# Kernel tuning notes

Measured on AMD Instinct MI355X. Metric: run time of the kernel, lower is better.

Reference implementation:

```python
import jax, jax.numpy as jnp
import numpy as np

B, N, DN = 8, 4096, 64
E = 1048576
H, DM = 128, 64   # message MLP: 2*DN -> H -> DM
HU, F = 128, 64   # node-update MLP: DN+DM -> HU -> F


def setup_inputs() -> dict:
    key = jax.random.key(0)
    ks = jax.random.split(key, 13)
    inp = {
        'node_feats': jax.random.normal(ks[0], (B, N, DN), dtype=jnp.float32),
        'edge_b': jax.random.randint(ks[1], (E,), 0, B, dtype=jnp.int32),
        'edge_src': jax.random.randint(ks[2], (E,), 0, N, dtype=jnp.int32),
        'edge_dst': jax.random.randint(ks[3], (E,), 0, N, dtype=jnp.int32),
        'edge_vals': jax.random.uniform(ks[4], (E,), dtype=jnp.float32),
        # message MLP params (Dense-relu, Dense-linear)
        'Wm1': jax.random.normal(ks[5], (2 * DN, H), dtype=jnp.float32) / np.sqrt(2 * DN),
        'bm1': jnp.zeros((H,), jnp.float32),
        'Wm2': jax.random.normal(ks[6], (H, DM), dtype=jnp.float32) / np.sqrt(H),
        'bm2': jnp.zeros((DM,), jnp.float32),
        # node-update MLP params
        'Wu1': jax.random.normal(ks[7], (DN + DM, HU), dtype=jnp.float32) / np.sqrt(DN + DM),
        'bu1': jnp.zeros((HU,), jnp.float32),
        'Wu2': jax.random.normal(ks[8], (HU, F), dtype=jnp.float32) / np.sqrt(HU),
        'bu2': jnp.zeros((F,), jnp.float32),
    }
    return inp


def reference(node_feats, edge_b, edge_src, edge_dst, edge_vals,
              Wm1, bm1, Wm2, bm2, Wu1, bu1, Wu2, bu2):
    # --- create messages: gather src/target feats per edge ---
    src_feats = node_feats[edge_b, edge_src]            # (E, DN)
    tgt_feats = node_feats[edge_b, edge_dst]            # (E, DN)
    feats = jnp.concatenate([src_feats, tgt_feats], axis=-1)  # (E, 2*DN)
    h = jax.nn.relu(feats @ Wm1 + bm1)
    messages = h @ Wm2 + bm2                            # (E, DM)

    # --- gather (scatter) messages: weighted ragged segment-mean ---
    weighted = messages * edge_vals[:, None]            # (E, DM)
    seg = edge_b * N + edge_src                          # rowids b*max_N + src
    sums = jax.ops.segment_sum(weighted, seg, num_segments=B * N)
    counts = jax.ops.segment_sum(jnp.ones((E,), weighted.dtype), seg,
                                 num_segments=B * N)
    gathered = sums / jnp.maximum(counts, 1.0)[:, None]  # mean; 0 for empty rows
    gathered = gathered.reshape(B, N, DM)

    # --- update nodes ---
    upd_in = jnp.concatenate([node_feats, gathered], axis=-1)  # (B, N, DN+DM)
    hu = jax.nn.relu(upd_in @ Wu1 + bu1)
    updated = hu @ Wu2 + bu2                            # (B, N, F)
    return updated
```

## Files before the change

### kernel.cpp

```cpp
#include <hip/hip_runtime.h>

#define NB 8
#define NN 4096
#define DNF 64
#define NEDGE 1048576
#define DM 64
#define FF 64

#define NBKT2 2048
#define SPB2 16
#define NXCD 8
#define SUBCAP 192
#define OVFCAP 65536

using f32x4 = __attribute__((ext_vector_type(4))) float;
using s16x8 = __attribute__((ext_vector_type(8))) short;

__device__ __forceinline__ unsigned short f2b(float f) {
    union { float f; unsigned u; } v; v.f = f;
    unsigned r = (v.u + 0x7fffu + ((v.u >> 16) & 1u)) >> 16;
    return (unsigned short)r;
}
__device__ __forceinline__ float uif(unsigned u) {
    union { unsigned u; float f; } v; v.u = u;
    return v.f;
}

__device__ __forceinline__ void pack_one(const float* __restrict__ W,
                                         unsigned short* __restrict__ out,
                                         int K, int Ncols, int idx) {
    int j = idx & 7;
    int lane = (idx >> 3) & 63;
    int frag = idx >> 9;
    int KS = K >> 5;
    int ks = frag % KS;
    int nt = frag / KS;
    int k = ks * 32 + ((lane >> 4) << 3) + j;
    int col = nt * 16 + (lane & 15);
    out[idx] = f2b(W[k * Ncols + col]);
}

__global__ void pack_all(const float* __restrict__ Wm1, const float* __restrict__ Wm2,
                         const float* __restrict__ Wu1, const float* __restrict__ Wu2,
                         unsigned short* __restrict__ Qw, unsigned short* __restrict__ Pw,
                         unsigned short* __restrict__ Wm2p,
                         unsigned short* __restrict__ Wu1p, unsigned short* __restrict__ Wu2p) {
    int idx = blockIdx.x * 256 + threadIdx.x;
    if (idx < 8192)        pack_one(Wm1,              Qw,   64, 128, idx);
    else if (idx < 16384)  pack_one(Wm1 + 64 * 128,   Pw,   64, 128, idx - 8192);
    else if (idx < 24576)  pack_one(Wm2,              Wm2p, 128, 64, idx - 16384);
    else if (idx < 40960)  pack_one(Wu1,              Wu1p, 128, 128, idx - 24576);
    else                   pack_one(Wu2,              Wu2p, 128, 64, idx - 40960);
}

__global__ void pack_weights(const float* __restrict__ W, unsigned short* __restrict__ out,
                             int K, int Ncols) {
    int idx = blockIdx.x * 256 + threadIdx.x;
    if (idx >= K * Ncols) return;
    pack_one(W, out, K, Ncols, idx);
}

__launch_bounds__(256, 4)
__global__ void precompute_pq(const float* __restrict__ X,
                              const unsigned short* __restrict__ Qw,
                              const unsigned short* __restrict__ Pw,
                              const float* __restrict__ b1,
                              unsigned short* __restrict__ Qp,
                              unsigned short* __restrict__ Pp) {
    __shared__ unsigned short A[64][72];
    const int tid = threadIdx.x;
    const int g0 = blockIdx.x * 64;
    for (int i = 0; i < 16; ++i) {
        int idx = i * 256 + tid;
        int node = idx >> 6;
        int f = idx & 63;
        A[node][f] = f2b(X[(size_t)(g0 + node) * DNF + f]);
    }
    __syncthreads();
    const int wave = tid >> 6, lane = tid & 63;
    const int lr = lane & 15, lq = lane >> 4;
    const int arow = wave * 16 + lr;
    s16x8 a[2];
#pragma unroll
    for (int ks = 0; ks < 2; ++ks)
        a[ks] = *reinterpret_cast<const s16x8*>(&A[arow][ks * 32 + lq * 8]);
#pragma unroll
    for (int nt = 0; nt < 8; ++nt) {
        f32x4 accQ = {0.f, 0.f, 0.f, 0.f};
        f32x4 accP = {0.f, 0.f, 0.f, 0.f};
#pragma unroll
        for (int ks = 0; ks < 2; ++ks) {
            s16x8 bq = *reinterpret_cast<const s16x8*>(&Qw[(((nt << 1) + ks) * 64 + lane) * 8]);
            s16x8 bp = *reinterpret_cast<const s16x8*>(&Pw[(((nt << 1) + ks) * 64 + lane) * 8]);
            accQ = __builtin_amdgcn_mfma_f32_16x16x32_bf16(a[ks], bq, accQ, 0, 0, 0);
            accP = __builtin_amdgcn_mfma_f32_16x16x32_bf16(a[ks], bp, accP, 0, 0, 0);
        }
        int col = nt * 16 + lr;
        float bias = b1[col];
#pragma unroll
        for (int j = 0; j < 4; ++j) {
            int row = g0 + wave * 16 + lq * 4 + j;
            Qp[(size_t)row * 128 + col] = f2b(accQ[j] + bias);
            Pp[(size_t)row * 128 + col] = f2b(accP[j]);
        }
    }
}

__launch_bounds__(256, 8)
__global__ void scatter_xcd(const int* __restrict__ eb, const int* __restrict__ esrc,
                            const int* __restrict__ edst, const float* __restrict__ evals,
                            unsigned* __restrict__ gcurX, unsigned* __restrict__ payslot,
                            unsigned* __restrict__ ovf_cnt, unsigned* __restrict__ ovf_seg,
                            unsigned* __restrict__ ovf_pay) {
    unsigned xcd;
    asm volatile("s_getreg_b32 %0, hwreg(HW_REG_XCC_ID)" : "=s"(xcd));
    xcd &= (NXCD - 1);
    const int t0 = blockIdx.x * 1024 + threadIdx.x;
    int seg[4]; unsigned pk[4];
#pragma unroll
    for (int k = 0; k < 4; ++k) {
        int e = t0 + k * 256;
        seg[k] = eb[e] * NN + esrc[e];
        unsigned wq = (unsigned)fminf(evals[e] * 8192.0f + 0.5f, 8191.0f);
        pk[k] = (unsigned)edst[e] | (wq << 12) | ((unsigned)(seg[k] & 15) << 25);
    }
    unsigned pos[4];
#pragma unroll
    for (int k = 0; k < 4; ++k)
        pos[k] = atomicAdd(&gcurX[xcd * NBKT2 + (seg[k] >> 4)], 1u);
#pragma unroll
    for (int k = 0; k < 4; ++k) {
        if (pos[k] < (unsigned)SUBCAP) {
            payslot[((size_t)(seg[k] >> 4) * NXCD + xcd) * SUBCAP + pos[k]] = pk[k];
        } else {
            unsigned o = atomicAdd(ovf_cnt, 1u);
            if (o < (unsigned)OVFCAP) { ovf_seg[o] = (unsigned)seg[k]; ovf_pay[o] = pk[k]; }
        }
    }
}

__launch_bounds__(256, 6)
__global__ void bucket16_fused(const unsigned short* __restrict__ Qp,
                               const unsigned short* __restrict__ Pp,
                               const unsigned* __restrict__ payslot,
                               const unsigned* __restrict__ gcurX,
                               const unsigned* __restrict__ ovf_cnt,
                               const unsigned* __restrict__ ovf_seg,
                               const unsigned* __restrict__ ovf_pay,
                               const unsigned short* __restrict__ Wm2p,
                               const float* __restrict__ b2m,
                               const float* __restrict__ X,
                               const unsigned short* __restrict__ Wu1p,
                               const float* __restrict__ bu1,
                               const unsigned short* __restrict__ Wu2p,
                               const float* __restrict__ bu2,
                               float* __restrict__ out) {
    __shared__ unsigned sorted[NXCD * SUBCAP];
    __shared__ unsigned short S[16][136];
    __shared__ unsigned short A1[16][136];
    __shared__ unsigned short Hs[16][136];
    __shared__ unsigned h[16];
    __shared__ unsigned offs[17];
    __shared__ unsigned curb[16];
    __shared__ unsigned cx[NXCD];
    __shared__ float SW[16], SC[16];
    const int tid = threadIdx.x, wv = tid >> 6, lane = tid & 63;
    const int bkt = blockIdx.x;
    const int node0 = bkt * SPB2;
    const int rowbase = (bkt >> 8) << 12;
    const unsigned novf = ovf_cnt[0];

#pragma unroll
    for (int i = 0; i < 4; ++i) {
        int idx = i * 256 + tid;
        int row = idx >> 6, f = idx & 63;
        A1[row][f] = f2b(X[(size_t)(node0 + row) * DNF + f]);
    }
    if (tid < 16) h[tid] = 0;
    if (tid < NXCD) cx[tid] = min(gcurX[tid * NBKT2 + bkt], (unsigned)SUBCAP);
    __syncthreads();
    for (int x = 0; x < NXCD; ++x) {
        unsigned c = cx[x];
        for (unsigned i = tid; i < c; i += 256) {
            unsigned v = payslot[((size_t)bkt * NXCD + x) * SUBCAP + i];
            atomicAdd(&h[(v >> 25) & 15u], 1u);
        }
    }
    __syncthreads();
    if (tid < 16) {
        int xx = (int)h[tid];
#pragma unroll
        for (int o = 1; o < 16; o <<= 1) {
            int y = __shfl_up(xx, o);
            if (tid >= o) xx += y;
        }
        offs[tid + 1] = (unsigned)xx;
        if (tid == 0) offs[0] = 0;
    }
    __syncthreads();
    if (tid < 16) curb[tid] = offs[tid];
    __syncthreads();
    for (int x = 0; x < NXCD; ++x) {
        unsigned c = cx[x];
        for (unsigned i = tid; i < c; i += 256) {
            unsigned v = payslot[((size_t)bkt * NXCD + x) * SUBCAP + i];
            unsigned pos = atomicAdd(&curb[(v >> 25) & 15u], 1u);
            sorted[pos] = v;
        }
    }
    __syncthreads();

    const unsigned* P32 = reinterpret_cast<const unsigned*>(Pp);
    const unsigned* Q32 = reinterpret_cast<const unsigned*>(Qp);
    for (int si = 0; si < 4; ++si) {
        const int lo = wv * 4 + si;
        const int seg = node0 + lo;
        const unsigned s0 = offs[lo], s1 = offs[lo + 1];
        unsigned qv = Q32[(size_t)seg * 64 + lane];
        float q0 = uif(qv << 16);
        float q1 = uif(qv & 0xffff0000u);
        float acc0 = 0.f, acc1 = 0.f, wsum = 0.f;
        unsigned scnt = s1 - s0;

        for (unsigned bse = s0; bse < s1; bse += 8) {
            unsigned pv[8]; float wf[8];
#pragma unroll
            for (int k = 0; k < 8; ++k) {
                unsigned idx = bse + (unsigned)k;
                unsigned c = (idx < s1) ? sorted[idx] : 0u;
                wf[k] = (float)((c >> 12) & 8191u) * (1.0f / 8192.0f);
                pv[k] = P32[(size_t)(rowbase + (int)(c & 0xfffu)) * 64 + lane];
            }
#pragma unroll
            for (int k = 0; k < 8; ++k) {
                float p0 = uif(pv[k] << 16);
                float p1 = uif(pv[k] & 0xffff0000u);
                acc0 = fmaf(wf[k], fmaxf(q0 + p0, 0.f), acc0);
                acc1 = fmaf(wf[k], fmaxf(q1 + p1, 0.f), acc1);
                wsum += wf[k];
            }
        }
        if (novf > 0) {
            unsigned ncl = min(novf, (unsigned)OVFCAP);
            for (unsigned i = 0; i < ncl; ++i) {
                if (ovf_seg[i] == (unsigned)seg) {
                    unsigned c = ovf_pay[i];
                    float w = (float)((c >> 12) & 8191u) * (1.0f / 8192.0f);
                    unsigned pv = P32[(size_t)(rowbase + (int)(c & 0xfffu)) * 64 + lane];
                    acc0 = fmaf(w, fmaxf(q0 + uif(pv << 16), 0.f), acc0);
                    acc1 = fmaf(w, fmaxf(q1 + uif(pv & 0xffff0000u), 0.f), acc1);
                    wsum += w;
                    scnt += 1;
                }
            }
        }
        unsigned sp = (unsigned)f2b(acc0) | ((unsigned)f2b(acc1) << 16);
        *reinterpret_cast<unsigned*>(&S[lo][2 * lane]) = sp;
        if (lane == 0) {
            SW[lo] = wsum;
            SC[lo] = 1.0f / (float)max(scnt, 1u);
        }
    }
    __syncthreads();

    const int lr = lane & 15, lq = lane >> 4;
    {
        s16x8 a[4];
#pragma unroll
        for (int ks = 0; ks < 4; ++ks)
            a[ks] = *reinterpret_cast<const s16x8*>(&S[lr][ks * 32 + lq * 8]);
        f32x4 acc = {0.f, 0.f, 0.f, 0.f};
#pragma unroll
        for (int ks = 0; ks < 4; ++ks) {
            s16x8 bf = *reinterpret_cast<const s16x8*>(&Wm2p[(((wv << 2) + ks) * 64 + lane) * 8]);
            acc = __builtin_amdgcn_mfma_f32_16x16x32_bf16(a[ks], bf, acc, 0, 0, 0);
        }
        float bb = b2m[wv * 16 + lr];
#pragma unroll
        for (int j = 0; j < 4; ++j) {
            int r = lq * 4 + j;
            float g = (acc[j] + SW[r] * bb) * SC[r];
            A1[r][64 + wv * 16 + lr] = f2b(g);
        }
    }
    __syncthreads();

    {
        s16x8 a1[4];
#pragma unroll
        for (int ks = 0; ks < 4; ++ks)
            a1[ks] = *reinterpret_cast<const s16x8*>(&A1[lr][ks * 32 + lq * 8]);
#pragma unroll
        for (int t = 0; t < 2; ++t) {
            int nt = wv * 2 + t;
            f32x4 acc = {0.f, 0.f, 0.f, 0.f};
#pragma unroll
            for (int ks = 0; ks < 4; ++ks) {
                s16x8 bf = *reinterpret_cast<const s16x8*>(&Wu1p[(((nt << 2) + ks) * 64 + lane) * 8]);
                acc = __builtin_amdgcn_mfma_f32_16x16x32_bf16(a1[ks], bf, acc, 0, 0, 0);
            }
            float bias = bu1[nt * 16 + lr];
#pragma unroll
            for (int j = 0; j < 4; ++j) {
                float hh = fmaxf(acc[j] + bias, 0.f);
                Hs[lq * 4 + j][nt * 16 + lr] = f2b(hh);
            }
        }
    }
    __syncthreads();

    {
        s16x8 a2[4];
#pragma unroll
        for (int ks = 0; ks < 4; ++ks)
            a2[ks] = *reinterpret_cast<const s16x8*>(&Hs[lr][ks * 32 + lq * 8]);
        f32x4 acc = {0.f, 0.f, 0.f, 0.f};
#pragma unroll
        for (int ks = 0; ks < 4; ++ks) {
            s16x8 bf = *reinterpret_cast<const s16x8*>(&Wu2p[(((wv << 2) + ks) * 64 + lane) * 8]);
            acc = __builtin_amdgcn_mfma_f32_16x16x32_bf16(a2[ks], bf, acc, 0, 0, 0);
        }
        float bias = bu2[wv * 16 + lr];
#pragma unroll
        for (int j = 0; j < 4; ++j)
            out[(size_t)(node0 + lq * 4 + j) * FF + wv * 16 + lr] = acc[j] + bias;
    }
}


template<int SCALE>
__launch_bounds__(256, 4)
__global__ void node_kernel(const float* __restrict__ node_feats,
                            const float* __restrict__ sums, const float* __restrict__ counts,
                            const unsigned short* __restrict__ W1p, const float* __restrict__ b1,
                            const unsigned short* __restrict__ W2p, const float* __restrict__ b2,
                            float* __restrict__ out) {
    __shared__ unsigned short A1[64][136];
    __shared__ unsigned short Hs[64][136];
    const int tid = threadIdx.x;
    const int g0 = blockIdx.x * 64;
    for (int i = 0; i < 16; ++i) {
        int idx = i * 256 + tid;
        int node = idx >> 6;
        int p = idx & 63;
        int g = g0 + node;
        float2 v;
        if (p < 32) {
            v = *reinterpret_cast<const float2*>(node_feats + (size_t)g * DNF + 2 * p);
        } else {
            float2 s = *reinterpret_cast<const float2*>(sums + (size_t)g * DM + 2 * p - 64);
            if (SCALE) {
                float scale = 1.0f / fmaxf(counts[g], 1.0f);
                s.x *= scale; s.y *= scale;
            }
            v = s;
        }
        unsigned packed = (unsigned)f2b(v.x) | ((unsigned)f2b(v.y) << 16);
        *reinterpret_cast<unsigned*>(&A1[node][2 * p]) = packed;
    }
    __syncthreads();
    const int wave = tid >> 6, lane = tid & 63;
    const int lr = lane & 15, lq = lane >> 4;
    const int arow = wave * 16 + lr;
    s16x8 a[4];
#pragma unroll
    for (int ks = 0; ks < 4; ++ks)
        a[ks] = *reinterpret_cast<const s16x8*>(&A1[arow][ks * 32 + lq * 8]);
#pragma unroll
    for (int nt = 0; nt < 8; ++nt) {
        f32x4 acc = {0.f, 0.f, 0.f, 0.f};
#pragma unroll
        for (int ks = 0; ks < 4; ++ks) {
            s16x8 bf = *reinterpret_cast<const s16x8*>(&W1p[(((nt << 2) + ks) * 64 + lane) * 8]);
            acc = __builtin_amdgcn_mfma_f32_16x16x32_bf16(a[ks], bf, acc, 0, 0, 0);
        }
        float bias = b1[nt * 16 + lr];
#pragma unroll
        for (int j = 0; j < 4; ++j) {
            float h = acc[j] + bias;
            h = h > 0.f ? h : 0.f;
            Hs[wave * 16 + lq * 4 + j][nt * 16 + lr] = f2b(h);
        }
    }
    s16x8 a2[4];
#pragma unroll
    for (int ks = 0; ks < 4; ++ks)
        a2[ks] = *reinterpret_cast<const s16x8*>(&Hs[arow][ks * 32 + lq * 8]);
#pragma unroll
    for (int nt = 0; nt < 4; ++nt) {
        f32x4 acc = {0.f, 0.f, 0.f, 0.f};
#pragma unroll
        for (int ks = 0; ks < 4; ++ks) {
            s16x8 bf = *reinterpret_cast<const s16x8*>(&W2p[(((nt << 2) + ks) * 64 + lane) * 8]);
            acc = __builtin_amdgcn_mfma_f32_16x16x32_bf16(a2[ks], bf, acc, 0, 0, 0);
        }
        float bias = b2[nt * 16 + lr];
#pragma unroll
        for (int j = 0; j < 4; ++j) {
            int g = g0 + wave * 16 + lq * 4 + j;
            out[(size_t)g * FF + nt * 16 + lr] = acc[j] + bias;
        }
    }
}

__launch_bounds__(256, 4)
__global__ void edge_kernel(const float* __restrict__ node_feats,
                            const int* __restrict__ eb, const int* __restrict__ esrc,
                            const int* __restrict__ edst, const float* __restrict__ evals,
                            const unsigned short* __restrict__ W1p, const float* __restrict__ b1,
                            const unsigned short* __restrict__ W2p, const float* __restrict__ b2,
                            float* __restrict__ sums, float* __restrict__ counts) {
    __shared__ unsigned short A1[64][136];
    __shared__ unsigned short Hs[64][136];
    const int tid = threadIdx.x;
    const int e0 = blockIdx.x * 64;
    if (tid < 64) {
        int e = e0 + tid;
        atomicAdd(&counts[eb[e] * NN + esrc[e]], 1.0f);
    }
    for (int i = 0; i < 16; ++i) {
        int idx = i * 256 + tid;
        int edge = idx >> 6;
        int p = idx & 63;
        int e = e0 + edge;
        int b = eb[e];
        const float* row;
        if (p < 32) row = node_feats + ((size_t)b * NN + esrc[e]) * DNF;
        else        row = node_feats + ((size_t)b * NN + edst[e]) * DNF - 64;
        float2 v = *reinterpret_cast<const float2*>(row + 2 * p);
        unsigned packed = (unsigned)f2b(v.x) | ((unsigned)f2b(v.y) << 16);
        *reinterpret_cast<unsigned*>(&A1[edge][2 * p]) = packed;
    }
    __syncthreads();
    const int wave = tid >> 6, lane = tid & 63;
    const int lr = lane & 15, lq = lane >> 4;
    const int arow = wave * 16 + lr;
    s16x8 a[4];
#pragma unroll
    for (int ks = 0; ks < 4; ++ks)
        a[ks] = *reinterpret_cast<const s16x8*>(&A1[arow][ks * 32 + lq * 8]);
#pragma unroll
    for (int nt = 0; nt < 8; ++nt) {
        f32x4 acc = {0.f, 0.f, 0.f, 0.f};
#pragma unroll
        for (int ks = 0; ks < 4; ++ks) {
            s16x8 bf = *reinterpret_cast<const s16x8*>(&W1p[(((nt << 2) + ks) * 64 + lane) * 8]);
            acc = __builtin_amdgcn_mfma_f32_16x16x32_bf16(a[ks], bf, acc, 0, 0, 0);
        }
        float bias = b1[nt * 16 + lr];
#pragma unroll
        for (int j = 0; j < 4; ++j) {
            float h = acc[j] + bias;
            h = h > 0.f ? h : 0.f;
            Hs[wave * 16 + lq * 4 + j][nt * 16 + lr] = f2b(h);
        }
    }
    s16x8 a2[4];
#pragma unroll
    for (int ks = 0; ks < 4; ++ks)
        a2[ks] = *reinterpret_cast<const s16x8*>(&Hs[arow][ks * 32 + lq * 8]);
    float ev[4]; int seg4[4];
#pragma unroll
    for (int j = 0; j < 4; ++j) {
        int r = e0 + wave * 16 + lq * 4 + j;
        ev[j] = evals[r];
        seg4[j] = eb[r] * NN + esrc[r];
    }
#pragma unroll
    for (int nt = 0; nt < 4; ++nt) {
        f32x4 acc = {0.f, 0.f, 0.f, 0.f};
#pragma unroll
        for (int ks = 0; ks < 4; ++ks) {
            s16x8 bf = *reinterpret_cast<const s16x8*>(&W2p[(((nt << 2) + ks) * 64 + lane) * 8]);
            acc = __builtin_amdgcn_mfma_f32_16x16x32_bf16(a2[ks], bf, acc, 0, 0, 0);
        }
        float bias = b2[nt * 16 + lr];
#pragma unroll
        for (int j = 0; j < 4; ++j) {
            float m = (acc[j] + bias) * ev[j];
            atomicAdd(&sums[(size_t)seg4[j] * DM + nt * 16 + lr], m);
        }
    }
}

extern "C" void kernel_launch(void* const* d_in, const int* in_sizes, int n_in,
                              void* d_out, int out_size, void* d_ws, size_t ws_size,
                              hipStream_t stream) {
    const float* node_feats = (const float*)d_in[0];
    const int*   eb    = (const int*)d_in[1];
    const int*   esrc  = (const int*)d_in[2];
    const int*   edst  = (const int*)d_in[3];
    const float* evals = (const float*)d_in[4];
    const float* Wm1 = (const float*)d_in[5];
    const float* bm1 = (const float*)d_in[6];
    const float* Wm2 = (const float*)d_in[7];
    const float* bm2 = (const float*)d_in[8];
    const float* Wu1 = (const float*)d_in[9];
    const float* bu1 = (const float*)d_in[10];
    const float* Wu2 = (const float*)d_in[11];
    const float* bu2 = (const float*)d_in[12];
    float* out = (float*)d_out;
    char* ws = (char*)d_ws;

    const size_t NEED = 30048384;
    if (ws_size >= NEED) {
        unsigned short* Qp      = (unsigned short*)(ws);
        unsigned short* Pp      = (unsigned short*)(ws + 8388608);
        unsigned*       payslot = (unsigned*)(ws + 16777216);
        unsigned*       gcurX   = (unsigned*)(ws + 29360128);
        unsigned*       ovf_cnt = (unsigned*)(ws + 29425664);
        unsigned*       ovf_seg = (unsigned*)(ws + 29425792);
        unsigned*       ovf_pay = (unsigned*)(ws + 29687936);
        unsigned short* Qw      = (unsigned short*)(ws + 29950080);
        unsigned short* Pw      = (unsigned short*)(ws + 29966464);
        unsigned short* Wu1p    = (unsigned short*)(ws + 29982848);
        unsigned short* Wu2p    = (unsigned short*)(ws + 30015616);
        unsigned short* Wm2p    = (unsigned short*)(ws + 30032000);

        hipMemsetAsync(gcurX, 0, 65536 + 128, stream);
        pack_all<<<192, 256, 0, stream>>>(Wm1, Wm2, Wu1, Wu2, Qw, Pw, Wm2p, Wu1p, Wu2p);
        precompute_pq<<<512, 256, 0, stream>>>(node_feats, Qw, Pw, bm1, Qp, Pp);
        scatter_xcd<<<NEDGE / 1024, 256, 0, stream>>>(eb, esrc, edst, evals,
                                                      gcurX, payslot, ovf_cnt, ovf_seg, ovf_pay);
        bucket16_fused<<<NBKT2, 256, 0, stream>>>(Qp, Pp, payslot, gcurX,
                                                  ovf_cnt, ovf_seg, ovf_pay,
                                                  Wm2p, bm2, node_feats,
                                                  Wu1p, bu1, Wu2p, bu2, out);
    } else {
        float* counts          = (float*)ws;
        unsigned short* W1p    = (unsigned short*)(ws + 131072);
        unsigned short* W2p    = (unsigned short*)(ws + 163840);
        unsigned short* Wu1p   = (unsigned short*)(ws + 180224);
        unsigned short* Wu2p   = (unsigned short*)(ws + 212992);
        hipMemsetAsync(d_out, 0, (size_t)out_size * sizeof(float), stream);
        hipMemsetAsync(counts, 0, 32768 * sizeof(float), stream);
        pack_weights<<<64, 256, 0, stream>>>(Wm1, W1p, 128, 128);
        pack_weights<<<32, 256, 0, stream>>>(Wm2, W2p, 128, 64);
        pack_weights<<<64, 256, 0, stream>>>(Wu1, Wu1p, 128, 128);
        pack_weights<<<32, 256, 0, stream>>>(Wu2, Wu2p, 128, 64);
        edge_kernel<<<NEDGE / 64, 256, 0, stream>>>(node_feats, eb, esrc, edst, evals,
                                                    W1p, bm1, W2p, bm2, out, counts);
        node_kernel<1><<<(NB * NN) / 64, 256, 0, stream>>>(node_feats, out, counts,
                                                           Wu1p, bu1, Wu2p, bu2, out);
    }
}
```

Measured before the change: 114.6 us.

## Scatter edges directly into per-segment per-XCD slots, drop in-block counting sort

The scatter kernel now bins each edge into a per-segment, per-XCD slot array with its own counter, in place of a per-16-segment bucket. The fused bucket kernel then skips the histogram, prefix scan and LDS counting sort. It only does a small 8-way prefix per segment and copies the payloads into a per-segment LDS array. This removes two payslot passes and the LDS atomics, at the cost of a much larger counter array (1 MB memset) and payload workspace. Edges beyond the per-slot capacity go to the overflow path, and the total per segment is limited to 128 by the LDS array.

```diff
diff --git a/kernel.cpp b/kernel.cpp
--- a/kernel.cpp
+++ b/kernel.cpp
@@ -7,10 +7,9 @@
 #define DM 64
 #define FF 64
 
+#define SPB2 16
 #define NBKT2 2048
-#define SPB2 16
 #define NXCD 8
-#define SUBCAP 192
 #define OVFCAP 65536
 
 using f32x4 = __attribute__((ext_vector_type(4))) float;
@@ -106,12 +105,13 @@
     }
 }
 
+template<int CAP>
 __launch_bounds__(256, 8)
-__global__ void scatter_xcd(const int* __restrict__ eb, const int* __restrict__ esrc,
-                            const int* __restrict__ edst, const float* __restrict__ evals,
-                            unsigned* __restrict__ gcurX, unsigned* __restrict__ payslot,
-                            unsigned* __restrict__ ovf_cnt, unsigned* __restrict__ ovf_seg,
-                            unsigned* __restrict__ ovf_pay) {
+__global__ void scatter_direct(const int* __restrict__ eb, const int* __restrict__ esrc,
+                               const int* __restrict__ edst, const float* __restrict__ evals,
+                               unsigned* __restrict__ gcur2, unsigned* __restrict__ payslot,
+                               unsigned* __restrict__ ovf_cnt, unsigned* __restrict__ ovf_seg,
+                               unsigned* __restrict__ ovf_pay) {
     unsigned xcd;
     asm volatile("s_getreg_b32 %0, hwreg(HW_REG_XCC_ID)" : "=s"(xcd));
     xcd &= (NXCD - 1);
@@ -122,16 +122,16 @@
         int e = t0 + k * 256;
         seg[k] = eb[e] * NN + esrc[e];
         unsigned wq = (unsigned)fminf(evals[e] * 8192.0f + 0.5f, 8191.0f);
-        pk[k] = (unsigned)edst[e] | (wq << 12) | ((unsigned)(seg[k] & 15) << 25);
+        pk[k] = (unsigned)edst[e] | (wq << 12);
     }
     unsigned pos[4];
 #pragma unroll
     for (int k = 0; k < 4; ++k)
-        pos[k] = atomicAdd(&gcurX[xcd * NBKT2 + (seg[k] >> 4)], 1u);
+        pos[k] = atomicAdd(&gcur2[(xcd << 15) + seg[k]], 1u);
 #pragma unroll
     for (int k = 0; k < 4; ++k) {
-        if (pos[k] < (unsigned)SUBCAP) {
-            payslot[((size_t)(seg[k] >> 4) * NXCD + xcd) * SUBCAP + pos[k]] = pk[k];
+        if (pos[k] < (unsigned)CAP) {
+            payslot[(size_t)((xcd << 15) + seg[k]) * CAP + pos[k]] = pk[k];
         } else {
             unsigned o = atomicAdd(ovf_cnt, 1u);
             if (o < (unsigned)OVFCAP) { ovf_seg[o] = (unsigned)seg[k]; ovf_pay[o] = pk[k]; }
@@ -139,11 +139,12 @@
     }
 }
 
+template<int CAP>
 __launch_bounds__(256, 6)
 __global__ void bucket16_fused(const unsigned short* __restrict__ Qp,
                                const unsigned short* __restrict__ Pp,
                                const unsigned* __restrict__ payslot,
-                               const unsigned* __restrict__ gcurX,
+                               const unsigned* __restrict__ gcur2,
                                const unsigned* __restrict__ ovf_cnt,
                                const unsigned* __restrict__ ovf_seg,
                                const unsigned* __restrict__ ovf_pay,
@@ -155,14 +156,13 @@
                                const unsigned short* __restrict__ Wu2p,
                                const float* __restrict__ bu2,
                                float* __restrict__ out) {
-    __shared__ unsigned sorted[NXCD * SUBCAP];
+    __shared__ unsigned pays[16][128];
     __shared__ unsigned short S[16][136];
     __shared__ unsigned short A1[16][136];
     __shared__ unsigned short Hs[16][136];
-    __shared__ unsigned h[16];
-    __shared__ unsigned offs[17];
-    __shared__ unsigned curb[16];
-    __shared__ unsigned cx[NXCD];
+    __shared__ unsigned pref[16][8];
+    __shared__ unsigned cl[16][8];
+    __shared__ unsigned cnts[16];
     __shared__ float SW[16], SC[16];
     const int tid = threadIdx.x, wv = tid >> 6, lane = tid & 63;
     const int bkt = blockIdx.x;
@@ -176,37 +176,28 @@
         int row = idx >> 6, f = idx & 63;
         A1[row][f] = f2b(X[(size_t)(node0 + row) * DNF + f]);
     }
-    if (tid < 16) h[tid] = 0;
-    if (tid < NXCD) cx[tid] = min(gcurX[tid * NBKT2 + bkt], (unsigned)SUBCAP);
-    __syncthreads();
-    for (int x = 0; x < NXCD; ++x) {
-        unsigned c = cx[x];
-        for (unsigned i = tid; i < c; i += 256) {
-            unsigned v = payslot[((size_t)bkt * NXCD + x) * SUBCAP + i];
-            atomicAdd(&h[(v >> 25) & 15u], 1u);
-        }
-    }
-    __syncthreads();
-    if (tid < 16) {
-        int xx = (int)h[tid];
-#pragma unroll
-        for (int o = 1; o < 16; o <<= 1) {
-            int y = __shfl_up(xx, o);
-            if (tid >= o) xx += y;
-        }
-        offs[tid + 1] = (unsigned)xx;
-        if (tid == 0) offs[0] = 0;
-    }
-    __syncthreads();
-    if (tid < 16) curb[tid] = offs[tid];
-    __syncthreads();
-    for (int x = 0; x < NXCD; ++x) {
-        unsigned c = cx[x];
-        for (unsigned i = tid; i < c; i += 256) {
-            unsigned v = payslot[((size_t)bkt * NXCD + x) * SUBCAP + i];
-            unsigned pos = atomicAdd(&curb[(v >> 25) & 15u], 1u);
-            sorted[pos] = v;
-        }
+    if (tid < 128) {
+        int lo = tid >> 3, x = tid & 7;
+        unsigned c = min(gcur2[(x << 15) + node0 + lo], (unsigned)CAP);
+        cl[lo][x] = c;
+        unsigned s = c;
+#pragma unroll
+        for (int o = 1; o < 8; o <<= 1) {
+            unsigned y = __shfl_up(s, o, 8);
+            if ((tid & 7) >= o) s += y;
+        }
+        pref[lo][x] = s - c;
+        if (x == 7) cnts[lo] = s;
+    }
+    __syncthreads();
+    {
+        int p = tid >> 1, sub = tid & 1;
+        int lo = p >> 3, x = p & 7;
+        unsigned c = cl[lo][x];
+        unsigned bse = pref[lo][x];
+        const unsigned* src = payslot + (size_t)((x << 15) + node0 + lo) * CAP;
+        for (unsigned i = sub; i < c; i += 2)
+            pays[lo][bse + i] = src[i];
     }
     __syncthreads();
 
@@ -215,19 +206,19 @@
     for (int si = 0; si < 4; ++si) {
         const int lo = wv * 4 + si;
         const int seg = node0 + lo;
-        const unsigned s0 = offs[lo], s1 = offs[lo + 1];
+        const unsigned s1 = cnts[lo];
         unsigned qv = Q32[(size_t)seg * 64 + lane];
         float q0 = uif(qv << 16);
         float q1 = uif(qv & 0xffff0000u);
         float acc0 = 0.f, acc1 = 0.f, wsum = 0.f;
-        unsigned scnt = s1 - s0;
-
-        for (unsigned bse = s0; bse < s1; bse += 8) {
+        unsigned scnt = s1;
+
+        for (unsigned bse = 0; bse < s1; bse += 8) {
             unsigned pv[8]; float wf[8];
 #pragma unroll
             for (int k = 0; k < 8; ++k) {
                 unsigned idx = bse + (unsigned)k;
-                unsigned c = (idx < s1) ? sorted[idx] : 0u;
+                unsigned c = (idx < s1) ? pays[lo][idx] : 0u;
                 wf[k] = (float)((c >> 12) & 8191u) * (1.0f / 8192.0f);
                 pv[k] = P32[(size_t)(rowbase + (int)(c & 0xfffu)) * 64 + lane];
             }
@@ -483,6 +474,38 @@
     }
 }
 
+template<int CAP>
+static void launch_direct(const float* node_feats, const int* eb, const int* esrc,
+                          const int* edst, const float* evals,
+                          const float* Wm1, const float* bm1, const float* Wm2, const float* bm2,
+                          const float* Wu1, const float* bu1, const float* Wu2, const float* bu2,
+                          float* out, char* ws, hipStream_t stream) {
+    const size_t PAYB = (size_t)NXCD * 32768 * CAP * 4;
+    unsigned short* Qp      = (unsigned short*)(ws);
+    unsigned short* Pp      = (unsigned short*)(ws + 8388608);
+    unsigned*       payslot = (unsigned*)(ws + 16777216);
+    char*           rest    = ws + 16777216 + PAYB;
+    unsigned*       gcur2   = (unsigned*)(rest);
+    unsigned*       ovf_cnt = (unsigned*)(rest + 1048576);
+    unsigned*       ovf_seg = (unsigned*)(rest + 1048704);
+    unsigned*       ovf_pay = (unsigned*)(rest + 1310848);
+    unsigned short* Qw      = (unsigned short*)(rest + 1572992);
+    unsigned short* Pw      = (unsigned short*)(rest + 1589376);
+    unsigned short* Wu1p    = (unsigned short*)(rest + 1605760);
+    unsigned short* Wu2p    = (unsigned short*)(rest + 1638528);
+    unsigned short* Wm2p    = (unsigned short*)(rest + 1654912);
+
+    hipMemsetAsync(gcur2, 0, 1048576 + 128, stream);
+    pack_all<<<192, 256, 0, stream>>>(Wm1, Wm2, Wu1, Wu2, Qw, Pw, Wm2p, Wu1p, Wu2p);
+    precompute_pq<<<512, 256, 0, stream>>>(node_feats, Qw, Pw, bm1, Qp, Pp);
+    scatter_direct<CAP><<<NEDGE / 1024, 256, 0, stream>>>(eb, esrc, edst, evals,
+                                                          gcur2, payslot, ovf_cnt, ovf_seg, ovf_pay);
+    bucket16_fused<CAP><<<NBKT2, 256, 0, stream>>>(Qp, Pp, payslot, gcur2,
+                                                   ovf_cnt, ovf_seg, ovf_pay,
+                                                   Wm2p, bm2, node_feats,
+                                                   Wu1p, bu1, Wu2p, bu2, out);
+}
+
 extern "C" void kernel_launch(void* const* d_in, const int* in_sizes, int n_in,
                               void* d_out, int out_size, void* d_ws, size_t ws_size,
                               hipStream_t stream) {
@@ -502,30 +525,15 @@
     float* out = (float*)d_out;
     char* ws = (char*)d_ws;
 
-    const size_t NEED = 30048384;
-    if (ws_size >= NEED) {
-        unsigned short* Qp      = (unsigned short*)(ws);
-        unsigned short* Pp      = (unsigned short*)(ws + 8388608);
-        unsigned*       payslot = (unsigned*)(ws + 16777216);
-        unsigned*       gcurX   = (unsigned*)(ws + 29360128);
-        unsigned*       ovf_cnt = (unsigned*)(ws + 29425664);
-        unsigned*       ovf_seg = (unsigned*)(ws + 29425792);
-        unsigned*       ovf_pay = (unsigned*)(ws + 29687936);
-        unsigned short* Qw      = (unsigned short*)(ws + 29950080);
-        unsigned short* Pw      = (unsigned short*)(ws + 29966464);
-        unsigned short* Wu1p    = (unsigned short*)(ws + 29982848);
-        unsigned short* Wu2p    = (unsigned short*)(ws + 30015616);
-        unsigned short* Wm2p    = (unsigned short*)(ws + 30032000);
-
-        hipMemsetAsync(gcurX, 0, 65536 + 128, stream);
-        pack_all<<<192, 256, 0, stream>>>(Wm1, Wm2, Wu1, Wu2, Qw, Pw, Wm2p, Wu1p, Wu2p);
-        precompute_pq<<<512, 256, 0, stream>>>(node_feats, Qw, Pw, bm1, Qp, Pp);
-        scatter_xcd<<<NEDGE / 1024, 256, 0, stream>>>(eb, esrc, edst, evals,
-                                                      gcurX, payslot, ovf_cnt, ovf_seg, ovf_pay);
-        bucket16_fused<<<NBKT2, 256, 0, stream>>>(Qp, Pp, payslot, gcurX,
-                                                  ovf_cnt, ovf_seg, ovf_pay,
-                                                  Wm2p, bm2, node_feats,
-                                                  Wu1p, bu1, Wu2p, bu2, out);
+    const size_t FIXED = 16777216 + 1671296;
+    const size_t NEED16 = FIXED + (size_t)NXCD * 32768 * 16 * 4;
+    const size_t NEED11 = FIXED + (size_t)NXCD * 32768 * 11 * 4;
+    if (ws_size >= NEED16) {
+        launch_direct<16>(node_feats, eb, esrc, edst, evals, Wm1, bm1, Wm2, bm2,
+                          Wu1, bu1, Wu2, bu2, out, ws, stream);
+    } else if (ws_size >= NEED11) {
+        launch_direct<11>(node_feats, eb, esrc, edst, evals, Wm1, bm1, Wm2, bm2,
+                          Wu1, bu1, Wu2, bu2, out, ws, stream);
     } else {
         float* counts          = (float*)ws;
         unsigned short* W1p    = (unsigned short*)(ws + 131072);
```

After: 133.6 us. 1.17x slower.
